# Optimization experiments

Measured on AMD Instinct MI355X. Metric: run time of the kernel, lower is better.

## Reference

```python
import jax, jax.numpy as jnp
import numpy as np

N, E, NC, F0, MID = 20000, 320000, 16, 67, 32
Y0 = 0.28209479177387814   # 1/(2*sqrt(pi)), real spherical harmonic l=0
C1 = 0.4886025119029199    # sqrt(3/(4*pi)),  real spherical harmonic l=1 coeff


def setup_inputs() -> dict:
    key = jax.random.key(0)
    ks = jax.random.split(key, 16)
    rn = lambda k, shape, s=1.0: jax.random.normal(k, shape, dtype=jnp.float32) * s
    return {
        "node_feats": rn(ks[0], (N, F0)),
        "pos": rn(ks[1], (N, 3)) * 3.0,
        "edge_w": jax.random.uniform(ks[2], (E, 2), dtype=jnp.float32),
        "lin1_W": rn(ks[5], (F0, F0), 1.0 / np.sqrt(F0)),
        "lin1_b": jnp.zeros((F0,), jnp.float32),
        "lin2_W": rn(ks[6], (F0, NC), 1.0 / np.sqrt(F0)),
        "lin2_b": jnp.zeros((NC,), jnp.float32),
        # 4 radial nets = 2 GConv layers x 2 degree pairs ((0,0),(0,1))
        "rW1": rn(ks[7], (4, 3, MID), 1.0 / np.sqrt(3)),
        "rb1": jnp.zeros((4, MID), jnp.float32),
        "ln1_g": jnp.ones((4, MID), jnp.float32),
        "ln1_b": jnp.zeros((4, MID), jnp.float32),
        "rW2": rn(ks[8], (4, MID, MID), 1.0 / np.sqrt(MID)),
        "rb2": jnp.zeros((4, MID), jnp.float32),
        "ln2_g": jnp.ones((4, MID), jnp.float32),
        "ln2_b": jnp.zeros((4, MID), jnp.float32),
        "rW3": rn(ks[9], (4, MID, NC * NC), 1.0 / np.sqrt(MID)),
        "rb3": jnp.zeros((4, NC * NC), jnp.float32),
        "Wself": rn(ks[10], (2, NC, NC), 1.0 / np.sqrt(NC)),
        "src": jax.random.randint(ks[3], (E,), 0, N),
        "dst": jax.random.randint(ks[4], (E,), 0, N),
    }


def _layer_norm(x, g, b, eps=1e-5):
    mu = jnp.mean(x, -1, keepdims=True)
    var = jnp.mean((x - mu) ** 2, -1, keepdims=True)
    return (x - mu) * jax.lax.rsqrt(var + eps) * g + b


def _forward(node_feats, pos, edge_w, lin1_W, lin1_b, lin2_W, lin2_b,
             rW1, rb1, ln1_g, ln1_b, rW2, rb2, ln2_g, ln2_b, rW3, rb3,
             Wself, src, dst):
    # node embedding: Linear -> ELU -> (dropout p=0) -> Linear -> [N, NC]
    h0 = jax.nn.elu(node_feats @ lin1_W + lin1_b) @ lin2_W + lin2_b

    # get_basis_and_r: relative positions, radial distance, SH basis (d_in=0)
    d = pos[dst] - pos[src]                                   # [E, 3]
    r = jnp.sqrt(jnp.sum(d * d, -1))                          # [E]
    rhat = d / jnp.maximum(r, 1e-8)[:, None]
    Y1 = C1 * rhat[:, jnp.array([1, 2, 0])]                   # [E, 3] (y, z, x order)
    feat = jnp.concatenate([edge_w, r[:, None]], -1)          # [E, edge_dim+1=3]

    deg = jax.ops.segment_sum(jnp.ones((E,), feat.dtype), dst, num_segments=N)
    inv_deg = jnp.where(deg > 0, 1.0 / jnp.maximum(deg, 1.0), 0.0)
    has_in = (deg > 0).astype(feat.dtype)

    def radial(i):
        h = jnp.maximum(_layer_norm(feat @ rW1[i] + rb1[i], ln1_g[i], ln1_b[i]), 0.0)
        h = jnp.maximum(_layer_norm(h @ rW2[i] + rb2[i], ln2_g[i], ln2_b[i]), 0.0)
        return (h @ rW3[i] + rb3[i]).reshape(E, NC, NC)       # [E, nc_out, nc_in]

    out1 = None
    for li in range(2):  # faithful to source bug: both layers read only degree-0 feats
        R00 = radial(2 * li)        # pairwise kernel (0->0), num_freq=1
        R01 = radial(2 * li + 1)    # pairwise kernel (0->1), num_freq=1
        s = h0[src]                                           # [E, NC] gather
        msg0 = Y0 * jnp.einsum('eoi,ei->eo', R00, s)          # [E, NC]
        msg1 = jnp.einsum('eoi,ei,em->eom', R01, s, Y1)       # [E, NC, 3]
        out0 = jax.ops.segment_sum(msg0, dst, num_segments=N) * inv_deg[:, None]
        out0 = out0 + has_in[:, None] * (h0 @ Wself[li].T)    # self-interaction (deg 0)
        out1 = jax.ops.segment_sum(msg1, dst, num_segments=N) * inv_deg[:, None, None]
        h0 = out0
    return h0[:, :, None], out1                               # {'0': [N,NC,1], '1': [N,NC,3]}


def reference(node_feats, pos, edge_w, lin1_W, lin1_b, lin2_W, lin2_b,
              rW1, rb1, ln1_g, ln1_b, rW2, rb2, ln2_g, ln2_b, rW3, rb3,
              Wself, src, dst):
    return _forward(node_feats, pos, edge_w, lin1_W, lin1_b, lin2_W, lin2_b,
                    rW1, rb1, ln1_g, ln1_b, rW2, rb2, ln2_g, ln2_b, rW3, rb3,
                    Wself, src, dst)
```

## Files before the change

kernel.cpp:

```cpp
#include <hip/hip_runtime.h>
#include <hip/hip_fp16.h>


#define Y0C 0.28209479177387814f
#define C1C 0.4886025119029199f

typedef _Float16 hv2 __attribute__((ext_vector_type(2)));

#if defined(__has_builtin)
#if __has_builtin(__builtin_amdgcn_fdot2)
#define FDOT2(a, b, c) __builtin_amdgcn_fdot2((a), (b), (c), false)
#endif
#endif
#ifndef FDOT2
#define FDOT2(a, b, c) ((c) + (float)(a).x * (float)(b).x + (float)(a).y * (float)(b).y)
#endif

static __device__ __forceinline__ unsigned h2u(__half2 h) {
    union { __half2 h; unsigned u; } x; x.h = h; return x.u;
}
static __device__ __forceinline__ __half2 u2h(unsigned u) {
    union { unsigned u; __half2 h; } x; x.u = u; return x.h;
}
static __device__ __forceinline__ hv2 u2hv(unsigned u) {
    union { unsigned u; hv2 h; } x; x.u = u; return x.h;
}
static __device__ __forceinline__ unsigned hv2u(hv2 h) {
    union { hv2 h; unsigned u; } x; x.h = h; return x.u;
}
static __device__ __forceinline__ hv2 f2hv(float a, float b) {
    hv2 r; r.x = (_Float16)a; r.y = (_Float16)b; return r;
}
static __device__ __forceinline__ float hbits2f(unsigned short s) {
    __half_raw r; r.x = s; return __half2float((__half)r);
}

struct RadialW {
    const float *W1, *b1, *g1, *gb1, *b2, *g2, *gb2;
    const unsigned* W2q;
};

__device__ __forceinline__ void radial_net_pk(float x0, float x1, float x2,
                                              RadialW rw, hv2* hvpk ) {
    float h[32];
#pragma unroll
    for (int j = 0; j < 32; ++j)
        h[j] = rw.b1[j] + x0 * rw.W1[j] + x1 * rw.W1[32 + j] + x2 * rw.W1[64 + j];
    float s0 = 0.f, s1 = 0.f, s2 = 0.f, s3 = 0.f;
#pragma unroll
    for (int p = 0; p < 8; ++p) {
        s0 += h[4 * p]; s1 += h[4 * p + 1]; s2 += h[4 * p + 2]; s3 += h[4 * p + 3];
    }
    float mu = ((s0 + s1) + (s2 + s3)) * 0.03125f;
    float v0 = 0.f, v1 = 0.f, v2 = 0.f, v3 = 0.f;
#pragma unroll
    for (int p = 0; p < 8; ++p) {
        float d0 = h[4 * p] - mu, d1 = h[4 * p + 1] - mu;
        float d2 = h[4 * p + 2] - mu, d3 = h[4 * p + 3] - mu;
        v0 = fmaf(d0, d0, v0); v1 = fmaf(d1, d1, v1);
        v2 = fmaf(d2, d2, v2); v3 = fmaf(d3, d3, v3);
    }
    float var = ((v0 + v1) + (v2 + v3)) * 0.03125f;
    float rs = rsqrtf(var + 1e-5f);
#pragma unroll
    for (int j = 0; j < 32; ++j)
        h[j] = fmaxf((h[j] - mu) * rs * rw.g1[j] + rw.gb1[j], 0.f);

    hv2 hp[16];
#pragma unroll
    for (int p = 0; p < 16; ++p) hp[p] = f2hv(h[2 * p], h[2 * p + 1]);

    float h2[32];
#pragma unroll
    for (int j = 0; j < 32; ++j) {
        float acc = rw.b2[j];
        const unsigned* __restrict__ wj = rw.W2q + j * 16;
#pragma unroll
        for (int kp = 0; kp < 16; ++kp)
            acc = FDOT2(hp[kp], u2hv(wj[kp]), acc);
        h2[j] = acc;
    }
    s0 = s1 = s2 = s3 = 0.f;
#pragma unroll
    for (int p = 0; p < 8; ++p) {
        s0 += h2[4 * p]; s1 += h2[4 * p + 1]; s2 += h2[4 * p + 2]; s3 += h2[4 * p + 3];
    }
    mu = ((s0 + s1) + (s2 + s3)) * 0.03125f;
    v0 = v1 = v2 = v3 = 0.f;
#pragma unroll
    for (int p = 0; p < 8; ++p) {
        float d0 = h2[4 * p] - mu, d1 = h2[4 * p + 1] - mu;
        float d2 = h2[4 * p + 2] - mu, d3 = h2[4 * p + 3] - mu;
        v0 = fmaf(d0, d0, v0); v1 = fmaf(d1, d1, v1);
        v2 = fmaf(d2, d2, v2); v3 = fmaf(d3, d3, v3);
    }
    var = ((v0 + v1) + (v2 + v3)) * 0.03125f;
    rs = rsqrtf(var + 1e-5f);
    float y[32];
#pragma unroll
    for (int j = 0; j < 32; ++j)
        y[j] = fmaxf((h2[j] - mu) * rs * rw.g2[j] + rw.gb2[j], 0.f);
#pragma unroll
    for (int p = 0; p < 16; ++p) hvpk[p] = f2hv(y[2 * p], y[2 * p + 1]);
}

__device__ __forceinline__ void contract_dot(const hv2* hvpk,
                                             const uint4* __restrict__ Um,
                                             const float* __restrict__ Ut,
                                             float* v ) {
    float4 t0 = ((const float4*)Ut)[0];
    float4 t1 = ((const float4*)Ut)[1];
    float4 t2 = ((const float4*)Ut)[2];
    float4 t3 = ((const float4*)Ut)[3];
    float tail[16] = {t0.x, t0.y, t0.z, t0.w, t1.x, t1.y, t1.z, t1.w,
                      t2.x, t2.y, t2.z, t2.w, t3.x, t3.y, t3.z, t3.w};
#pragma unroll
    for (int o = 0; o < 16; ++o) {
        uint4 q0 = Um[o * 4];
        uint4 q1 = Um[o * 4 + 1];
        uint4 q2 = Um[o * 4 + 2];
        uint4 q3 = Um[o * 4 + 3];
        float acc = tail[o];
        acc = FDOT2(hvpk[0],  u2hv(q0.x), acc);
        acc = FDOT2(hvpk[1],  u2hv(q0.y), acc);
        acc = FDOT2(hvpk[2],  u2hv(q0.z), acc);
        acc = FDOT2(hvpk[3],  u2hv(q0.w), acc);
        acc = FDOT2(hvpk[4],  u2hv(q1.x), acc);
        acc = FDOT2(hvpk[5],  u2hv(q1.y), acc);
        acc = FDOT2(hvpk[6],  u2hv(q1.z), acc);
        acc = FDOT2(hvpk[7],  u2hv(q1.w), acc);
        acc = FDOT2(hvpk[8],  u2hv(q2.x), acc);
        acc = FDOT2(hvpk[9],  u2hv(q2.y), acc);
        acc = FDOT2(hvpk[10], u2hv(q2.z), acc);
        acc = FDOT2(hvpk[11], u2hv(q2.w), acc);
        acc = FDOT2(hvpk[12], u2hv(q3.x), acc);
        acc = FDOT2(hvpk[13], u2hv(q3.y), acc);
        acc = FDOT2(hvpk[14], u2hv(q3.z), acc);
        acc = FDOT2(hvpk[15], u2hv(q3.w), acc);
        v[o] = acc;
    }
}

__global__ __launch_bounds__(256) void k_fuse1(
    const float* __restrict__ nf, const float* __restrict__ W1,
    const float* __restrict__ b1, float* __restrict__ t, int N,
    int nbC, int nbEmb,
    const float* __restrict__ rW3, const float* __restrict__ rW2,
    unsigned* __restrict__ Wp, unsigned* __restrict__ Wq,
    const int* __restrict__ src, const int* __restrict__ dst,
    int* __restrict__ cntd, int* __restrict__ cnts,
    int* __restrict__ posd, int* __restrict__ poss, int E) {
    int b = blockIdx.x;
    int q = b >> 2;
    bool isCount = ((b & 3) == 3) && (q < nbC);
    if (isCount) {
        int e = q * 256 + threadIdx.x;
        if (e >= E) return;
        posd[e] = atomicAdd(cntd + dst[e], 1);
        poss[e] = atomicAdd(cnts + src[e], 1);
        return;
    }
    int dense = b - min(q, nbC);
    if (dense >= nbEmb) {
        int tt = (dense - nbEmb) * 256 + threadIdx.x;
        if (tt < 3 * 256) {
            int ni = tt >> 8;
            int net = (ni == 0) ? 0 : ni + 1;
            int r = tt & 255;
            int i = r >> 4, o = r & 15;
            const float* __restrict__ W3n = rW3 + (size_t)net * 8192;
            unsigned* __restrict__ dp = Wp + (size_t)ni * 4608 + (size_t)(i * 16 + o) * 18;
#pragma unroll
            for (int kp = 0; kp < 16; ++kp) {
                float a = W3n[(2 * kp) * 256 + o * 16 + i];
                float bv = W3n[(2 * kp + 1) * 256 + o * 16 + i];
                dp[kp] = h2u(__floats2half2_rn(a, bv));
            }
        } else if (tt < 3 * 256 + 3 * 512) {
            int r = tt - 3 * 256;
            int ni = r / 512;
            int net = (ni == 0) ? 0 : ni + 1;
            int jk = r - ni * 512;
            int j = jk >> 4, kp = jk & 15;
            const float* __restrict__ W2n = rW2 + (size_t)net * 1024;
            Wq[ni * 512 + j * 16 + kp] =
                h2u(__floats2half2_rn(W2n[(2 * kp) * 32 + j],
                                      W2n[(2 * kp + 1) * 32 + j]));
        }
        return;
    }
    int idx = dense * 256 + threadIdx.x;
    if (idx >= N * 67) return;
    int n = idx / 67, j = idx - n * 67;
    const float* __restrict__ x = nf + (size_t)n * 67;
    const float* __restrict__ w = W1 + j;
    float a0 = b1[j], a1 = 0.f, a2 = 0.f, a3 = 0.f;
#pragma unroll
    for (int i = 0; i < 64; i += 4) {
        a0 = fmaf(x[i],     w[(size_t)i * 67],       a0);
        a1 = fmaf(x[i + 1], w[(size_t)(i + 1) * 67], a1);
        a2 = fmaf(x[i + 2], w[(size_t)(i + 2) * 67], a2);
        a3 = fmaf(x[i + 3], w[(size_t)(i + 3) * 67], a3);
    }
    a0 = fmaf(x[64], w[64 * 67], a0);
    a1 = fmaf(x[65], w[65 * 67], a1);
    a2 = fmaf(x[66], w[66 * 67], a2);
    float s = (a0 + a1) + (a2 + a3);
    t[idx] = (s > 0.f) ? s : expm1f(s);
}

__global__ __launch_bounds__(1024) void k_fuse2(
    const int* __restrict__ cntd, int* __restrict__ rsd,
    const int* __restrict__ cnts, int* __restrict__ rss, int N,
    const float* __restrict__ t, const float* __restrict__ W2,
    const float* __restrict__ b2, float* __restrict__ h0) {
    if (blockIdx.x < 2) {
        const int* __restrict__ c = (blockIdx.x == 0) ? cntd : cnts;
        int* __restrict__ rs      = (blockIdx.x == 0) ? rsd  : rss;
        int chunk = (N + 1023) >> 10;
        int lo = (int)threadIdx.x * chunk;
        int sum = 0;
        for (int j = 0; j < chunk; ++j) { int i = lo + j; sum += (i < N) ? c[i] : 0; }
        __shared__ int ps[1024];
        ps[threadIdx.x] = sum;
        __syncthreads();
        for (int off = 1; off < 1024; off <<= 1) {
            int v = (threadIdx.x >= (unsigned)off) ? ps[threadIdx.x - off] : 0;
            __syncthreads();
            ps[threadIdx.x] += v;
            __syncthreads();
        }
        int run = threadIdx.x ? ps[threadIdx.x - 1] : 0;
        if (threadIdx.x == 0) rs[0] = 0;
        for (int j = 0; j < chunk; ++j) {
            int i = lo + j;
            if (i < N) { run += c[i]; rs[i + 1] = run; }
        }
        return;
    }
    int idx = (blockIdx.x - 2) * 1024 + threadIdx.x;
    if (idx >= N * 16) return;
    int n = idx >> 4, c = idx & 15;
    const float* __restrict__ x = t + (size_t)n * 67;
    const float* __restrict__ w = W2 + c;
    float a0 = b2[c], a1 = 0.f, a2 = 0.f, a3 = 0.f;
#pragma unroll
    for (int i = 0; i < 64; i += 4) {
        a0 = fmaf(x[i],     w[(size_t)i * 16],       a0);
        a1 = fmaf(x[i + 1], w[(size_t)(i + 1) * 16], a1);
        a2 = fmaf(x[i + 2], w[(size_t)(i + 2) * 16], a2);
        a3 = fmaf(x[i + 3], w[(size_t)(i + 3) * 16], a3);
    }
    a0 = fmaf(x[64], w[64 * 16], a0);
    a1 = fmaf(x[65], w[65 * 16], a1);
    a2 = fmaf(x[66], w[66 * 16], a2);
    h0[idx] = (a0 + a1) + (a2 + a3);
}

__device__ __forceinline__ void u2_body(
    unsigned* WL, int nbase, const float* __restrict__ h,
    const float* __restrict__ b3, unsigned* __restrict__ Um,
    float* __restrict__ Ut, int N) {
    int o = threadIdx.x & 15;
    int pr = threadIdx.x >> 4;
    int n0 = nbase + pr * 2;
    int n1 = n0 + 1;
    bool ok0 = n0 < N, ok1 = n1 < N;
    int m0 = ok0 ? n0 : 0, m1 = ok1 ? n1 : 0;

    const float* __restrict__ bo = b3 + o * 16;
    float tA = 0.f, tB = 0.f;
    __half2 hhA[16], hhB[16];
    {
        const float4* hp = (const float4*)(h + (size_t)m0 * 16);
#pragma unroll
        for (int q = 0; q < 4; ++q) {
            float4 hv = hp[q];
            tA += hv.x * bo[4 * q] + hv.y * bo[4 * q + 1]
                + hv.z * bo[4 * q + 2] + hv.w * bo[4 * q + 3];
            hhA[4 * q]     = __floats2half2_rn(hv.x, hv.x);
            hhA[4 * q + 1] = __floats2half2_rn(hv.y, hv.y);
            hhA[4 * q + 2] = __floats2half2_rn(hv.z, hv.z);
            hhA[4 * q + 3] = __floats2half2_rn(hv.w, hv.w);
        }
    }
    {
        const float4* hp = (const float4*)(h + (size_t)m1 * 16);
#pragma unroll
        for (int q = 0; q < 4; ++q) {
            float4 hv = hp[q];
            tB += hv.x * bo[4 * q] + hv.y * bo[4 * q + 1]
                + hv.z * bo[4 * q + 2] + hv.w * bo[4 * q + 3];
            hhB[4 * q]     = __floats2half2_rn(hv.x, hv.x);
            hhB[4 * q + 1] = __floats2half2_rn(hv.y, hv.y);
            hhB[4 * q + 2] = __floats2half2_rn(hv.z, hv.z);
            hhB[4 * q + 3] = __floats2half2_rn(hv.w, hv.w);
        }
    }

    __half2 accA[16], accB[16];
#pragma unroll
    for (int p = 0; p < 16; ++p) {
        accA[p] = __floats2half2_rn(0.f, 0.f);
        accB[p] = __floats2half2_rn(0.f, 0.f);
    }

#pragma unroll
    for (int i = 0; i < 16; ++i) {
        const uint2* __restrict__ row = (const uint2*)(WL + i * 288 + o * 18);
        __half2 ha = hhA[i], hb = hhB[i];
#pragma unroll
        for (int q = 0; q < 8; ++q) {
            uint2 w = row[q];
            accA[2 * q]     = __hfma2(ha, u2h(w.x), accA[2 * q]);
            accA[2 * q + 1] = __hfma2(ha, u2h(w.y), accA[2 * q + 1]);
            accB[2 * q]     = __hfma2(hb, u2h(w.x), accB[2 * q]);
            accB[2 * q + 1] = __hfma2(hb, u2h(w.y), accB[2 * q + 1]);
        }
    }

    if (ok0) {
        uint4* du = (uint4*)(Um + ((size_t)(n0 * 16 + o)) * 16);
#pragma unroll
        for (int q = 0; q < 4; ++q)
            du[q] = make_uint4(h2u(accA[4 * q]), h2u(accA[4 * q + 1]),
                               h2u(accA[4 * q + 2]), h2u(accA[4 * q + 3]));
        Ut[n0 * 16 + o] = tA;
    }
    if (ok1) {
        uint4* du = (uint4*)(Um + ((size_t)(n1 * 16 + o)) * 16);
#pragma unroll
        for (int q = 0; q < 4; ++q)
            du[q] = make_uint4(h2u(accB[4 * q]), h2u(accB[4 * q + 1]),
                               h2u(accB[4 * q + 2]), h2u(accB[4 * q + 3]));
        Ut[n1 * 16 + o] = tB;
    }
}

__global__ __launch_bounds__(256) void k_fuse3(
    const float* __restrict__ h, const unsigned* __restrict__ Wp,
    const float* __restrict__ b3, unsigned* __restrict__ Um,
    float* __restrict__ Ut, int nbU, int N,
    const float* __restrict__ pos, const float* __restrict__ ew,
    const int* __restrict__ src, const int* __restrict__ dst,
    const int* __restrict__ rsd, const int* __restrict__ rss,
    const int* __restrict__ posd, const int* __restrict__ poss,
    float4* __restrict__ edgeS, uint2* __restrict__ y1d,
    int* __restrict__ s2d, int E) {
    __shared__ unsigned WL[4608];
    if (blockIdx.x < (unsigned)nbU) {
        for (int j = threadIdx.x; j < 4608; j += 256) WL[j] = Wp[j];
        __syncthreads();
        u2_body(WL, blockIdx.x * 32, h, b3, Um, Ut, N);
        return;
    }
    int e = (blockIdx.x - nbU) * 256 + threadIdx.x;
    if (e >= E) return;
    int s = src[e], d = dst[e];
    float dx = pos[3 * d]     - pos[3 * s];
    float dy = pos[3 * d + 1] - pos[3 * s + 1];
    float dz = pos[3 * d + 2] - pos[3 * s + 2];
    float r = sqrtf(dx * dx + dy * dy + dz * dz);
    float im = 1.f / fmaxf(r, 1e-8f);
    int ts = rss[s] + poss[e];
    int td = rsd[d] + posd[e];
    s2d[ts] = td;
    edgeS[ts] = make_float4(ew[2 * e], ew[2 * e + 1], r, __int_as_float(s));
    y1d[td] = make_uint2(h2u(__floats2half2_rn(C1C * dy * im, C1C * dz * im)),
                         h2u(__floats2half2_rn(C1C * dx * im, 0.f)));
}

__global__ __launch_bounds__(256) void k_u2(
    const float* __restrict__ h, const unsigned* __restrict__ Wp,
    const float* __restrict__ b3A, const float* __restrict__ b3B,
    unsigned* __restrict__ Um0, float* __restrict__ Ut0,
    unsigned* __restrict__ Um1, float* __restrict__ Ut1,
    int wpA, int nbPerNet, int N) {
    __shared__ unsigned WL[4608];
    int netSel = blockIdx.x / nbPerNet;
    int nbase = (blockIdx.x - netSel * nbPerNet) * 32;
    const unsigned* __restrict__ g = Wp + (size_t)(wpA + netSel) * 4608;
    for (int j = threadIdx.x; j < 4608; j += 256) WL[j] = g[j];
    __syncthreads();
    u2_body(WL, nbase, h, netSel ? b3B : b3A,
            netSel ? Um1 : Um0, netSel ? Ut1 : Ut0, N);
}

__global__ __launch_bounds__(256) void k_edgeL0(
    const float4* __restrict__ edgeS, const int* __restrict__ s2d, RadialW ra,
    const uint4* __restrict__ UmA, const float* __restrict__ UtA,
    unsigned short* __restrict__ msg , int E) {
    int t = blockIdx.x * blockDim.x + threadIdx.x;
    if (t >= E) return;
    float4 a = edgeS[t];
    int sn = __float_as_int(a.w);
    hv2 hv[16];
    float v[16];
    radial_net_pk(a.x, a.y, a.z, ra, hv);
    contract_dot(hv, UmA + (size_t)sn * 64, UtA + (size_t)sn * 16, v);
    int td = s2d[t];
    uint4* m = (uint4*)(msg + (size_t)td * 16);
    m[0] = make_uint4(hv2u(f2hv(v[0], v[1])),  hv2u(f2hv(v[2], v[3])),
                      hv2u(f2hv(v[4], v[5])),  hv2u(f2hv(v[6], v[7])));
    m[1] = make_uint4(hv2u(f2hv(v[8], v[9])),  hv2u(f2hv(v[10], v[11])),
                      hv2u(f2hv(v[12], v[13])), hv2u(f2hv(v[14], v[15])));
}

__global__ __launch_bounds__(256) void k_edgeL1(
    const float4* __restrict__ edgeS, const int* __restrict__ s2d,
    RadialW ra, RadialW rb,
    const uint4* __restrict__ UmA, const float* __restrict__ UtA,
    const uint4* __restrict__ UmB, const float* __restrict__ UtB,
    unsigned short* __restrict__ msg , int nbE, int E) {
    int half = (blockIdx.x >= (unsigned)nbE) ? 1 : 0;
    int t = (blockIdx.x - half * nbE) * blockDim.x + threadIdx.x;
    if (t >= E) return;
    float4 a = edgeS[t];
    int sn = __float_as_int(a.w);
    RadialW rw = half ? rb : ra;
    const uint4* __restrict__ Um = half ? UmB : UmA;
    const float* __restrict__ Ut = half ? UtB : UtA;
    hv2 hv[16];
    float v[16];
    radial_net_pk(a.x, a.y, a.z, rw, hv);
    contract_dot(hv, Um + (size_t)sn * 64, Ut + (size_t)sn * 16, v);
    int td = s2d[t];
    uint4* m = (uint4*)(msg + (size_t)td * 32 + half * 16);
    m[0] = make_uint4(hv2u(f2hv(v[0], v[1])),  hv2u(f2hv(v[2], v[3])),
                      hv2u(f2hv(v[4], v[5])),  hv2u(f2hv(v[6], v[7])));
    m[1] = make_uint4(hv2u(f2hv(v[8], v[9])),  hv2u(f2hv(v[10], v[11])),
                      hv2u(f2hv(v[12], v[13])), hv2u(f2hv(v[14], v[15])));
}

__global__ void k_reduce0(const unsigned short* __restrict__ msg,
                          const int* __restrict__ rowstart,
                          const float* __restrict__ h, const float* __restrict__ Wself,
                          float* __restrict__ out, int N) {
    int idx = blockIdx.x * blockDim.x + threadIdx.x;
    if (idx >= N * 16) return;
    int n = idx >> 4, o = idx & 15;
    int s = rowstart[n], t1 = rowstart[n + 1];
    float acc0 = 0.f, acc1 = 0.f;
    int t = s;
    for (; t + 1 < t1; t += 2) {
        acc0 += hbits2f(msg[(size_t)t * 16 + o]);
        acc1 += hbits2f(msg[(size_t)(t + 1) * 16 + o]);
    }
    if (t < t1) acc0 += hbits2f(msg[(size_t)t * 16 + o]);
    float acc = acc0 + acc1;
    int d = t1 - s;
    float invd = (d > 0) ? 1.f / (float)d : 0.f;
    float hi   = (d > 0) ? 1.f : 0.f;
    const float* __restrict__ hn = h + (size_t)n * 16;
    const float* __restrict__ w  = Wself + o * 16;
    float self = 0.f;
#pragma unroll
    for (int c = 0; c < 16; ++c) self += hn[c] * w[c];
    out[idx] = Y0C * acc * invd + hi * self;
}

__global__ void k_reduce1(const unsigned short* __restrict__ msg,
                          const uint2* __restrict__ y1d,
                          const int* __restrict__ rowstart,
                          const float* __restrict__ h, const float* __restrict__ Wself,
                          float* __restrict__ out0, float* __restrict__ out1, int N) {
    int idx = blockIdx.x * blockDim.x + threadIdx.x;
    if (idx >= N * 16) return;
    int n = idx >> 4, o = idx & 15;
    int s = rowstart[n], t1 = rowstart[n + 1];
    float a0 = 0.f, ax = 0.f, ay = 0.f, az = 0.f;
    float b0 = 0.f, bx = 0.f, by = 0.f, bz = 0.f;
    int t = s;
    for (; t + 1 < t1; t += 2) {
        const unsigned short* rowA = msg + (size_t)t * 32;
        const unsigned short* rowB = msg + (size_t)(t + 1) * 32;
        uint2 yva = y1d[t];
        uint2 yvb = y1d[t + 1];
        a0 += hbits2f(rowA[o]);
        b0 += hbits2f(rowB[o]);
        float pa = hbits2f(rowA[16 + o]);
        float pb = hbits2f(rowB[16 + o]);
        ax = fmaf(pa, hbits2f((unsigned short)yva.x), ax);
        ay = fmaf(pa, hbits2f((unsigned short)(yva.x >> 16)), ay);
        az = fmaf(pa, hbits2f((unsigned short)yva.y), az);
        bx = fmaf(pb, hbits2f((unsigned short)yvb.x), bx);
        by = fmaf(pb, hbits2f((unsigned short)(yvb.x >> 16)), by);
        bz = fmaf(pb, hbits2f((unsigned short)yvb.y), bz);
    }
    if (t < t1) {
        const unsigned short* rowA = msg + (size_t)t * 32;
        uint2 yva = y1d[t];
        a0 += hbits2f(rowA[o]);
        float pa = hbits2f(rowA[16 + o]);
        ax = fmaf(pa, hbits2f((unsigned short)yva.x), ax);
        ay = fmaf(pa, hbits2f((unsigned short)(yva.x >> 16)), ay);
        az = fmaf(pa, hbits2f((unsigned short)yva.y), az);
    }
    a0 += b0; ax += bx; ay += by; az += bz;
    int d = t1 - s;
    float invd = (d > 0) ? 1.f / (float)d : 0.f;
    float hi   = (d > 0) ? 1.f : 0.f;
    const float* __restrict__ hn = h + (size_t)n * 16;
    const float* __restrict__ w  = Wself + o * 16;
    float self = 0.f;
#pragma unroll
    for (int c = 0; c < 16; ++c) self += hn[c] * w[c];
    out0[idx] = Y0C * a0 * invd + hi * self;
    out1[(size_t)idx * 3]     = ax * invd;
    out1[(size_t)idx * 3 + 1] = ay * invd;
    out1[(size_t)idx * 3 + 2] = az * invd;
}

extern "C" void kernel_launch(void* const* d_in, const int* in_sizes, int n_in,
                              void* d_out, int out_size, void* d_ws, size_t ws_size,
                              hipStream_t stream) {
    (void)n_in; (void)out_size; (void)ws_size;
    const float* node_feats = (const float*)d_in[0];
    const float* pos    = (const float*)d_in[1];
    const float* edge_w = (const float*)d_in[2];
    const float* lin1_W = (const float*)d_in[3];
    const float* lin1_b = (const float*)d_in[4];
    const float* lin2_W = (const float*)d_in[5];
    const float* lin2_b = (const float*)d_in[6];
    const float* rW1    = (const float*)d_in[7];
    const float* rb1    = (const float*)d_in[8];
    const float* ln1_g  = (const float*)d_in[9];
    const float* ln1_b  = (const float*)d_in[10];
    const float* rW2    = (const float*)d_in[11];
    const float* rb2    = (const float*)d_in[12];
    const float* ln2_g  = (const float*)d_in[13];
    const float* ln2_b  = (const float*)d_in[14];
    const float* rW3    = (const float*)d_in[15];
    const float* rb3    = (const float*)d_in[16];
    const float* Wself  = (const float*)d_in[17];
    const int*   src    = (const int*)d_in[18];
    const int*   dst    = (const int*)d_in[19];

    const int N = in_sizes[1] / 3;
    const int E = in_sizes[18];

    char* ws = (char*)d_ws;
    size_t off = 0;
    auto carve = [&](size_t bytes) -> char* {
        char* p = ws + off;
        off = (off + bytes + 255) & ~(size_t)255;
        return p;
    };
    float* h0   = (float*)carve((size_t)N * 16 * 4);
    float* h1   = (float*)carve((size_t)N * 16 * 4);
    int*   cntd = (int*)carve((size_t)N * 4);
    int*   cnts = (int*)carve((size_t)N * 4);
    int*   rsd  = (int*)carve((size_t)(N + 1) * 4);
    int*   rss  = (int*)carve((size_t)(N + 1) * 4);
    int*   s2d  = (int*)carve((size_t)E * 4);
    float4* edgeS = (float4*)carve((size_t)E * 16);
    uint2*  y1d   = (uint2*)carve((size_t)E * 8);
    unsigned* UaM = (unsigned*)carve((size_t)N * 16 * 64);
    float*    UaT = (float*)carve((size_t)N * 16 * 4);
    unsigned* UbM = (unsigned*)carve((size_t)N * 16 * 64);
    float*    UbT = (float*)carve((size_t)N * 16 * 4);
    unsigned* Wp  = (unsigned*)carve((size_t)3 * 4608 * 4);
    unsigned* Wq  = (unsigned*)carve((size_t)3 * 512 * 4);
    unsigned short* msg = (unsigned short*)carve((size_t)E * 32 * 2);
    float* tmb = (float*)msg;
    int* posd = (int*)((char*)msg + (8u << 20));
    int* poss = (int*)((char*)msg + (14u << 20));

    auto nb = [](int n) { return (n + 255) / 256; };
    const int nbE = nb(E);
    const int nbU = (N + 31) / 32;
    const int nbE1 = nb(N * 67);
    int nbF1 = nbE1 + 9 + nbE;
    if (nbF1 < 4 * nbE) nbF1 = 4 * nbE;

    hipMemsetAsync(cntd, 0, (size_t)((char*)cnts - (char*)cntd) + (size_t)N * 4, stream);

    k_fuse1<<<nbF1, 256, 0, stream>>>(node_feats, lin1_W, lin1_b, tmb, N,
                                      nbE, nbE1, rW3, rW2, Wp, Wq,
                                      src, dst, cntd, cnts, posd, poss, E);
    k_fuse2<<<2 + (N * 16 + 1023) / 1024, 1024, 0, stream>>>(
        cntd, rsd, cnts, rss, N, tmb, lin2_W, lin2_b, h0);
    k_fuse3<<<nbU + nbE, 256, 0, stream>>>(h0, Wp, rb3, UaM, UaT, nbU, N,
                                           pos, edge_w, src, dst, rsd, rss,
                                           posd, poss, edgeS, y1d, s2d, E);

    auto rnet = [&](int net, int ni) -> RadialW {
        RadialW r;
        r.W1 = rW1 + net * 96;   r.b1 = rb1 + net * 32;
        r.g1 = ln1_g + net * 32; r.gb1 = ln1_b + net * 32;
        r.b2 = rb2 + net * 32;
        r.g2 = ln2_g + net * 32; r.gb2 = ln2_b + net * 32;
        r.W2q = Wq + ni * 512;
        return r;
    };

    k_edgeL0<<<nbE, 256, 0, stream>>>(edgeS, s2d, rnet(0, 0), (const uint4*)UaM, UaT,
                                      msg, E);
    k_reduce0<<<nb(N * 16), 256, 0, stream>>>(msg, rsd, h0, Wself, h1, N);

    k_u2<<<2 * nbU, 256, 0, stream>>>(h1, Wp, rb3 + 2 * 256, rb3 + 3 * 256,
                                      UaM, UaT, UbM, UbT, 1, nbU, N);
    k_edgeL1<<<2 * nbE, 256, 0, stream>>>(edgeS, s2d, rnet(2, 1), rnet(3, 2),
                                          (const uint4*)UaM, UaT,
                                          (const uint4*)UbM, UbT, msg, nbE, E);
    float* out0 = (float*)d_out;
    float* out1 = (float*)d_out + (size_t)N * 16;
    k_reduce1<<<nb(N * 16), 256, 0, stream>>>(msg, y1d, rsd, h1, Wself + 256,
                                              out0, out1, N);
}
```

Before: 311.2 us.

## Interleave per-node U matrix and tail, halve count blocks, interleave U2 blocks

Packs each node's 16x16 half-precision U matrix and its 16-float tail into one contiguous 272-word record, so the edge kernels read a single region per source node instead of two separate arrays. The atomic counting blocks in k_fuse1 now handle two edges per thread, cutting the number of count blocks in half. In k_fuse3 the U2 blocks are interleaved with the edge-prep blocks (every third block) instead of all being launched first, to balance the mix of work across the GPU. Risks include different atomic contention patterns and an unaligned total grid when nbU is large relative to the edge blocks.

```diff
diff --git a/kernel.cpp b/kernel.cpp
--- a/kernel.cpp
+++ b/kernel.cpp
@@ -105,9 +105,10 @@
 }
 
 __device__ __forceinline__ void contract_dot(const hv2* hvpk,
-                                             const uint4* __restrict__ Um,
-                                             const float* __restrict__ Ut,
+                                             const unsigned* __restrict__ Up,
                                              float* v ) {
+    const uint4* __restrict__ Um = (const uint4*)Up;
+    const float* __restrict__ Ut = (const float*)(Up + 256);
     float4 t0 = ((const float4*)Ut)[0];
     float4 t1 = ((const float4*)Ut)[1];
     float4 t2 = ((const float4*)Ut)[2];
@@ -154,10 +155,16 @@
     int q = b >> 2;
     bool isCount = ((b & 3) == 3) && (q < nbC);
     if (isCount) {
-        int e = q * 256 + threadIdx.x;
-        if (e >= E) return;
-        posd[e] = atomicAdd(cntd + dst[e], 1);
-        poss[e] = atomicAdd(cnts + src[e], 1);
+        int e0 = q * 256 + threadIdx.x;
+        int e1 = e0 + nbC * 256;
+        if (e0 < E) {
+            posd[e0] = atomicAdd(cntd + dst[e0], 1);
+            poss[e0] = atomicAdd(cnts + src[e0], 1);
+        }
+        if (e1 < E) {
+            posd[e1] = atomicAdd(cntd + dst[e1], 1);
+            poss[e1] = atomicAdd(cnts + src[e1], 1);
+        }
         return;
     }
     int dense = b - min(q, nbC);
@@ -259,8 +266,7 @@
 
 __device__ __forceinline__ void u2_body(
     unsigned* WL, int nbase, const float* __restrict__ h,
-    const float* __restrict__ b3, unsigned* __restrict__ Um,
-    float* __restrict__ Ut, int N) {
+    const float* __restrict__ b3, unsigned* __restrict__ Um, int N) {
     int o = threadIdx.x & 15;
     int pr = threadIdx.x >> 4;
     int n0 = nbase + pr * 2;
@@ -320,27 +326,28 @@
     }
 
     if (ok0) {
-        uint4* du = (uint4*)(Um + ((size_t)(n0 * 16 + o)) * 16);
+        unsigned* base = Um + (size_t)n0 * 272;
+        uint4* du = (uint4*)(base + o * 16);
 #pragma unroll
         for (int q = 0; q < 4; ++q)
             du[q] = make_uint4(h2u(accA[4 * q]), h2u(accA[4 * q + 1]),
                                h2u(accA[4 * q + 2]), h2u(accA[4 * q + 3]));
-        Ut[n0 * 16 + o] = tA;
+        ((float*)(base + 256))[o] = tA;
     }
     if (ok1) {
-        uint4* du = (uint4*)(Um + ((size_t)(n1 * 16 + o)) * 16);
+        unsigned* base = Um + (size_t)n1 * 272;
+        uint4* du = (uint4*)(base + o * 16);
 #pragma unroll
         for (int q = 0; q < 4; ++q)
             du[q] = make_uint4(h2u(accB[4 * q]), h2u(accB[4 * q + 1]),
                                h2u(accB[4 * q + 2]), h2u(accB[4 * q + 3]));
-        Ut[n1 * 16 + o] = tB;
+        ((float*)(base + 256))[o] = tB;
     }
 }
 
 __global__ __launch_bounds__(256) void k_fuse3(
     const float* __restrict__ h, const unsigned* __restrict__ Wp,
-    const float* __restrict__ b3, unsigned* __restrict__ Um,
-    float* __restrict__ Ut, int nbU, int N,
+    const float* __restrict__ b3, unsigned* __restrict__ Um, int nbU, int N,
     const float* __restrict__ pos, const float* __restrict__ ew,
     const int* __restrict__ src, const int* __restrict__ dst,
     const int* __restrict__ rsd, const int* __restrict__ rss,
@@ -348,13 +355,17 @@
     float4* __restrict__ edgeS, uint2* __restrict__ y1d,
     int* __restrict__ s2d, int E) {
     __shared__ unsigned WL[4608];
-    if (blockIdx.x < (unsigned)nbU) {
+    int b = blockIdx.x;
+    int k = b / 3;
+    bool isU2 = ((b % 3) == 2) && (k < nbU);
+    if (isU2) {
         for (int j = threadIdx.x; j < 4608; j += 256) WL[j] = Wp[j];
         __syncthreads();
-        u2_body(WL, blockIdx.x * 32, h, b3, Um, Ut, N);
+        u2_body(WL, k * 32, h, b3, Um, N);
         return;
     }
-    int e = (blockIdx.x - nbU) * 256 + threadIdx.x;
+    int dense = b - min(b / 3, nbU);
+    int e = dense * 256 + threadIdx.x;
     if (e >= E) return;
     int s = src[e], d = dst[e];
     float dx = pos[3 * d]     - pos[3 * s];
@@ -373,8 +384,7 @@
 __global__ __launch_bounds__(256) void k_u2(
     const float* __restrict__ h, const unsigned* __restrict__ Wp,
     const float* __restrict__ b3A, const float* __restrict__ b3B,
-    unsigned* __restrict__ Um0, float* __restrict__ Ut0,
-    unsigned* __restrict__ Um1, float* __restrict__ Ut1,
+    unsigned* __restrict__ Um0, unsigned* __restrict__ Um1,
     int wpA, int nbPerNet, int N) {
     __shared__ unsigned WL[4608];
     int netSel = blockIdx.x / nbPerNet;
@@ -382,13 +392,12 @@
     const unsigned* __restrict__ g = Wp + (size_t)(wpA + netSel) * 4608;
     for (int j = threadIdx.x; j < 4608; j += 256) WL[j] = g[j];
     __syncthreads();
-    u2_body(WL, nbase, h, netSel ? b3B : b3A,
-            netSel ? Um1 : Um0, netSel ? Ut1 : Ut0, N);
+    u2_body(WL, nbase, h, netSel ? b3B : b3A, netSel ? Um1 : Um0, N);
 }
 
 __global__ __launch_bounds__(256) void k_edgeL0(
     const float4* __restrict__ edgeS, const int* __restrict__ s2d, RadialW ra,
-    const uint4* __restrict__ UmA, const float* __restrict__ UtA,
+    const unsigned* __restrict__ UmA,
     unsigned short* __restrict__ msg , int E) {
     int t = blockIdx.x * blockDim.x + threadIdx.x;
     if (t >= E) return;
@@ -397,7 +406,7 @@
     hv2 hv[16];
     float v[16];
     radial_net_pk(a.x, a.y, a.z, ra, hv);
-    contract_dot(hv, UmA + (size_t)sn * 64, UtA + (size_t)sn * 16, v);
+    contract_dot(hv, UmA + (size_t)sn * 272, v);
     int td = s2d[t];
     uint4* m = (uint4*)(msg + (size_t)td * 16);
     m[0] = make_uint4(hv2u(f2hv(v[0], v[1])),  hv2u(f2hv(v[2], v[3])),
@@ -409,8 +418,7 @@
 __global__ __launch_bounds__(256) void k_edgeL1(
     const float4* __restrict__ edgeS, const int* __restrict__ s2d,
     RadialW ra, RadialW rb,
-    const uint4* __restrict__ UmA, const float* __restrict__ UtA,
-    const uint4* __restrict__ UmB, const float* __restrict__ UtB,
+    const unsigned* __restrict__ UmA, const unsigned* __restrict__ UmB,
     unsigned short* __restrict__ msg , int nbE, int E) {
     int half = (blockIdx.x >= (unsigned)nbE) ? 1 : 0;
     int t = (blockIdx.x - half * nbE) * blockDim.x + threadIdx.x;
@@ -418,12 +426,11 @@
     float4 a = edgeS[t];
     int sn = __float_as_int(a.w);
     RadialW rw = half ? rb : ra;
-    const uint4* __restrict__ Um = half ? UmB : UmA;
-    const float* __restrict__ Ut = half ? UtB : UtA;
+    const unsigned* __restrict__ Um = half ? UmB : UmA;
     hv2 hv[16];
     float v[16];
     radial_net_pk(a.x, a.y, a.z, rw, hv);
-    contract_dot(hv, Um + (size_t)sn * 64, Ut + (size_t)sn * 16, v);
+    contract_dot(hv, Um + (size_t)sn * 272, v);
     int td = s2d[t];
     uint4* m = (uint4*)(msg + (size_t)td * 32 + half * 16);
     m[0] = make_uint4(hv2u(f2hv(v[0], v[1])),  hv2u(f2hv(v[2], v[3])),
@@ -555,10 +562,8 @@
     int*   s2d  = (int*)carve((size_t)E * 4);
     float4* edgeS = (float4*)carve((size_t)E * 16);
     uint2*  y1d   = (uint2*)carve((size_t)E * 8);
-    unsigned* UaM = (unsigned*)carve((size_t)N * 16 * 64);
-    float*    UaT = (float*)carve((size_t)N * 16 * 4);
-    unsigned* UbM = (unsigned*)carve((size_t)N * 16 * 64);
-    float*    UbT = (float*)carve((size_t)N * 16 * 4);
+    unsigned* UaM = (unsigned*)carve((size_t)N * 272 * 4);
+    unsigned* UbM = (unsigned*)carve((size_t)N * 272 * 4);
     unsigned* Wp  = (unsigned*)carve((size_t)3 * 4608 * 4);
     unsigned* Wq  = (unsigned*)carve((size_t)3 * 512 * 4);
     unsigned short* msg = (unsigned short*)carve((size_t)E * 32 * 2);
@@ -570,17 +575,18 @@
     const int nbE = nb(E);
     const int nbU = (N + 31) / 32;
     const int nbE1 = nb(N * 67);
-    int nbF1 = nbE1 + 9 + nbE;
-    if (nbF1 < 4 * nbE) nbF1 = 4 * nbE;
+    const int nbC = nb((E + 1) / 2);
+    int nbF1 = nbE1 + 9 + nbC;
+    if (nbF1 < 4 * nbC) nbF1 = 4 * nbC;
 
     hipMemsetAsync(cntd, 0, (size_t)((char*)cnts - (char*)cntd) + (size_t)N * 4, stream);
 
     k_fuse1<<<nbF1, 256, 0, stream>>>(node_feats, lin1_W, lin1_b, tmb, N,
-                                      nbE, nbE1, rW3, rW2, Wp, Wq,
+                                      nbC, nbE1, rW3, rW2, Wp, Wq,
                                       src, dst, cntd, cnts, posd, poss, E);
     k_fuse2<<<2 + (N * 16 + 1023) / 1024, 1024, 0, stream>>>(
         cntd, rsd, cnts, rss, N, tmb, lin2_W, lin2_b, h0);
-    k_fuse3<<<nbU + nbE, 256, 0, stream>>>(h0, Wp, rb3, UaM, UaT, nbU, N,
+    k_fuse3<<<nbU + nbE, 256, 0, stream>>>(h0, Wp, rb3, UaM, nbU, N,
                                            pos, edge_w, src, dst, rsd, rss,
                                            posd, poss, edgeS, y1d, s2d, E);
 
@@ -594,15 +600,13 @@
         return r;
     };
 
-    k_edgeL0<<<nbE, 256, 0, stream>>>(edgeS, s2d, rnet(0, 0), (const uint4*)UaM, UaT,
-                                      msg, E);
+    k_edgeL0<<<nbE, 256, 0, stream>>>(edgeS, s2d, rnet(0, 0), UaM, msg, E);
     k_reduce0<<<nb(N * 16), 256, 0, stream>>>(msg, rsd, h0, Wself, h1, N);
 
     k_u2<<<2 * nbU, 256, 0, stream>>>(h1, Wp, rb3 + 2 * 256, rb3 + 3 * 256,
-                                      UaM, UaT, UbM, UbT, 1, nbU, N);
+                                      UaM, UbM, 1, nbU, N);
     k_edgeL1<<<2 * nbE, 256, 0, stream>>>(edgeS, s2d, rnet(2, 1), rnet(3, 2),
-                                          (const uint4*)UaM, UaT,
-                                          (const uint4*)UbM, UbT, msg, nbE, E);
+                                          UaM, UbM, msg, nbE, E);
     float* out0 = (float*)d_out;
     float* out1 = (float*)d_out + (size_t)N * 16;
     k_reduce1<<<nb(N * 16), 256, 0, stream>>>(msg, y1d, rsd, h1, Wself + 256,
```

Result: no change. 317.0 us (+1.9%).
